# Performance work log

Measured on AMD Instinct MI355X. Metric: run time of the kernel, lower is better.

The kernel has to match this reference:

```python
import jax, jax.numpy as jnp
import numpy as np
import math

B, S, HID = 1, 2048, 4096
NH, NKV, HD = 32, 8, 128
N_REP = NH // NKV
ROPE_THETA = 10000.0


def setup_inputs() -> dict:
    key = jax.random.key(0)
    ks = jax.random.split(key, 5)
    hidden_states = jax.random.normal(ks[0], (B, S, HID), dtype=jnp.float32)
    # additive causal mask: 0 on/below diagonal, -1e9 above
    causal = jnp.triu(jnp.full((S, S), -1e9, dtype=jnp.float32), k=1)
    attention_mask = causal[None, None, :, :]
    wq = jax.random.normal(ks[1], (HID, NH * HD), dtype=jnp.float32) * 0.02
    wk = jax.random.normal(ks[2], (HID, NKV * HD), dtype=jnp.float32) * 0.02
    wv = jax.random.normal(ks[3], (HID, NKV * HD), dtype=jnp.float32) * 0.02
    wo = jax.random.normal(ks[4], (NH * HD, HID), dtype=jnp.float32) * 0.02
    return {"hidden_states": hidden_states, "attention_mask": attention_mask,
            "wq": wq, "wk": wk, "wv": wv, "wo": wo}


def _rope_cos_sin(seq_len, head_dim, base, dtype):
    inv_freq = 1.0 / (base ** (jnp.arange(0, head_dim, 2, dtype=jnp.float32) / head_dim))
    t = jnp.arange(seq_len, dtype=jnp.float32)
    freqs = jnp.outer(t, inv_freq)          # [S, HD/2]
    emb = jnp.concatenate([freqs, freqs], axis=-1)  # [S, HD]
    return jnp.cos(emb).astype(dtype), jnp.sin(emb).astype(dtype)


def _rotate_interleaved(x):
    # pairs (x0,x1) -> (-x1, x0), interleaved (matches torch stack/reshape trick)
    xp = x.reshape(*x.shape[:-1], -1, 2)
    return jnp.stack([-xp[..., 1], xp[..., 0]], axis=-1).reshape(x.shape)


def reference(hidden_states, attention_mask, wq, wk, wv, wo):
    b, s, _ = hidden_states.shape
    q = (hidden_states @ wq).reshape(b, s, NH, HD).transpose(0, 2, 1, 3)   # [B,NH,S,HD]
    k = (hidden_states @ wk).reshape(b, s, NKV, HD).transpose(0, 2, 1, 3)  # [B,NKV,S,HD]
    v = (hidden_states @ wv).reshape(b, s, NKV, HD).transpose(0, 2, 1, 3)

    cos, sin = _rope_cos_sin(s, HD, ROPE_THETA, hidden_states.dtype)
    cos = cos[None, None, :, :]  # broadcast over batch and heads
    sin = sin[None, None, :, :]
    q = q * cos + _rotate_interleaved(q) * sin
    k = k * cos + _rotate_interleaved(k) * sin

    # repeat_kv: [B,NKV,S,HD] -> [B,NH,S,HD]
    k = jnp.repeat(k, N_REP, axis=1)
    v = jnp.repeat(v, N_REP, axis=1)

    scores = jnp.einsum('bhqd,bhkd->bhqk', q, k) / math.sqrt(HD)
    scores = scores + attention_mask
    attn = jax.nn.softmax(scores.astype(jnp.float32), axis=-1).astype(q.dtype)
    out = jnp.einsum('bhqk,bhkd->bhqd', attn, v)          # [B,NH,S,HD]
    out = out.transpose(0, 2, 1, 3).reshape(b, s, NH * HD)
    return out @ wo
```

## Files before the change

### kernel.cpp

```cpp
#include <hip/hip_runtime.h>

#define S_LEN 2048
#define HID 4096
#define NH 32
#define NKV 8
#define HD 128
#define KVW 1024
#define NQKV 6144

typedef _Float16 f16;
typedef _Float16 f16x8 __attribute__((ext_vector_type(8)));
typedef _Float16 f16x4 __attribute__((ext_vector_type(4)));
typedef float f32x4 __attribute__((ext_vector_type(4)));
typedef float f32x16 __attribute__((ext_vector_type(16)));
typedef unsigned int u32;
typedef u32 u32x4 __attribute__((ext_vector_type(4)));

__device__ __forceinline__ void gll16(const void* g, void* lds) {
  __builtin_amdgcn_global_load_lds((const __attribute__((address_space(1))) void*)g,
                                   (__attribute__((address_space(3))) void*)lds, 16, 0, 0);
}

template<int N> __device__ __forceinline__ void vmwait() {
  if constexpr (N == 0) asm volatile("s_waitcnt vmcnt(0)" ::: "memory");
  else if constexpr (N == 3) asm volatile("s_waitcnt vmcnt(3)" ::: "memory");
  else if constexpr (N == 4) asm volatile("s_waitcnt vmcnt(4)" ::: "memory");
  else static_assert(N == 0 || N == 3 || N == 4, "add vmcnt case");
}

__global__ void k_cast(const float* __restrict__ src, f16* __restrict__ dst) {
  size_t i = ((size_t)blockIdx.x * blockDim.x + threadIdx.x) * 8;
  float4 a = *(const float4*)(src + i);
  float4 b = *(const float4*)(src + i + 4);
  f16x8 o = { (f16)a.x, (f16)a.y, (f16)a.z, (f16)a.w,
              (f16)b.x, (f16)b.y, (f16)b.z, (f16)b.w };
  *(f16x8*)(dst + i) = o;
}

__global__ void k_trig(float4* __restrict__ trig) {
  int id = blockIdx.x * blockDim.x + threadIdx.x;
  int s = id >> 6, i = id & 63;
  int j0 = 2 * i, j1 = 2 * i + 1;
  float f0 = powf(10000.f, -(float)(j0 & 63) / 64.f);
  float f1 = powf(10000.f, -(float)(j1 & 63) / 64.f);
  float a0 = (float)s * f0, a1 = (float)s * f1;
  trig[id] = make_float4(cosf(a0), cosf(a1), sinf(a0), sinf(a1));
}

__global__ __launch_bounds__(256) void k_wprep(
    const float* __restrict__ wq, const float* __restrict__ wk,
    const float* __restrict__ wv, const float* __restrict__ wo,
    f16* __restrict__ Wt, f16* __restrict__ Wot)
{
  __shared__ float tile[32][33];
  int bid = blockIdx.x;
  const float* src; f16* dst; int N; int r;
  if (bid < 16384)      { src = wq; dst = Wt;                          N = 4096; r = bid; }
  else if (bid < 20480) { src = wk; dst = Wt + (size_t)4096 * 4096;    N = 1024; r = bid - 16384; }
  else if (bid < 24576) { src = wv; dst = Wt + (size_t)5120 * 4096;    N = 1024; r = bid - 20480; }
  else                  { src = wo; dst = Wot;                         N = 4096; r = bid - 24576; }
  int tpr = N >> 5;
  int kb = (r / tpr) * 32, nb = (r % tpr) * 32;
  int t = threadIdx.x;
  {
    int kl = t >> 3, ng = t & 7;
    float4 v = *(const float4*)(src + (size_t)(kb + kl) * N + nb + ng * 4);
    tile[kl][ng * 4 + 0] = v.x; tile[kl][ng * 4 + 1] = v.y;
    tile[kl][ng * 4 + 2] = v.z; tile[kl][ng * 4 + 3] = v.w;
  }
  __syncthreads();
  {
    int nl = t >> 3, kg = t & 7;
    f16x4 o = { (f16)tile[kg * 4 + 0][nl], (f16)tile[kg * 4 + 1][nl],
                (f16)tile[kg * 4 + 2][nl], (f16)tile[kg * 4 + 3][nl] };
    *(f16x4*)(dst + (size_t)(nb + nl) * HID + kb + kg * 4) = o;
  }
}

extern __shared__ char smem[];

template<int MODE, int MF, int NF, int WM, int WN>
__global__ __launch_bounds__(WM * WN * 64, 2) void k_gemm4(
    const f16* __restrict__ A, const f16* __restrict__ Bt,
    f16* __restrict__ Qr, f16* __restrict__ Kr, f16* __restrict__ Vt,
    const float4* __restrict__ trig, float* __restrict__ Cout)
{
  constexpr int NTHR = WM * WN * 64;
  constexpr int BM = WM * MF * 16;
  constexpr int BN = WN * NF * 16;
  constexpr int ABYTES = BM * 128;
  constexpr int BBYTES = BN * 128;
  constexpr int RPC = NTHR / 8;
  constexpr int ACALLS = BM / RPC;
  constexpr int BCALLS = BN / RPC;
  constexpr int NT = 64;

  const int tid = threadIdx.x, ln = tid & 63, w = tid >> 6;
  const int la = ln & 15, lg = ln >> 4;
  const int wr = w / WN, wc = w % WN;
  const int m0 = blockIdx.y * BM, n0 = blockIdx.x * BN;

  const char* asrc[ACALLS];
  const char* bsrc[BCALLS];
  int adst[ACALLS > BCALLS ? ACALLS : BCALLS];
#pragma unroll
  for (int c = 0; c < ACALLS; ++c) {
    int r = c * RPC + (tid >> 3);
    int g = (tid & 7) ^ (r & 7);
    asrc[c] = (const char*)A + ((size_t)(m0 + r) * HID + (size_t)g * 8) * 2;
    adst[c] = c * NTHR * 16 + tid * 16;
  }
#pragma unroll
  for (int c = 0; c < BCALLS; ++c) {
    int r = c * RPC + (tid >> 3);
    int g = (tid & 7) ^ (r & 7);
    bsrc[c] = (const char*)Bt + ((size_t)(n0 + (r >= BN ? r - BN : r)) * HID + (size_t)g * 8) * 2;
  }

  char* const Bbase = smem + 2 * ABYTES;
  f32x4 acc[MF][NF] = {};

#pragma unroll
  for (int c = 0; c < ACALLS; ++c) gll16(asrc[c], smem + adst[c]);
#pragma unroll
  for (int c = 0; c < BCALLS; ++c) gll16(bsrc[c], Bbase + adst[c]);
#pragma unroll
  for (int c = 0; c < BCALLS; ++c) gll16(bsrc[c] + 128, Bbase + BBYTES + adst[c]);
  vmwait<BCALLS>();
  __builtin_amdgcn_s_barrier();

  for (int t = 0; t < NT; ++t) {
    if (t + 1 < NT) {
      char* sa = smem + ((t + 1) & 1) * ABYTES;
#pragma unroll
      for (int c = 0; c < ACALLS; ++c) gll16(asrc[c] + (size_t)(t + 1) * 128, sa + adst[c]);
    }
    if (t + 2 < NT) {
      char* sb = Bbase + ((t + 2) % 3) * BBYTES;
#pragma unroll
      for (int c = 0; c < BCALLS; ++c) gll16(bsrc[c] + (size_t)(t + 2) * 128, sb + adst[c]);
    }
    const char* sa = smem + (t & 1) * ABYTES;
    const char* sb = Bbase + (t % 3) * BBYTES;
#pragma unroll
    for (int ks = 0; ks < 2; ++ks) {
      f16x8 af[MF], bf[NF];
#pragma unroll
      for (int i = 0; i < MF; ++i) {
        int rl = wr * MF * 16 + i * 16 + la;
        af[i] = *(const f16x8*)(sa + rl * 128 + (((ks * 4 + lg) ^ (rl & 7)) * 16));
      }
#pragma unroll
      for (int n = 0; n < NF; ++n) {
        int rb = wc * NF * 16 + n * 16 + la;
        bf[n] = *(const f16x8*)(sb + rb * 128 + (((ks * 4 + lg) ^ (rb & 7)) * 16));
      }
      __builtin_amdgcn_s_setprio(1);
#pragma unroll
      for (int i = 0; i < MF; ++i)
#pragma unroll
        for (int n = 0; n < NF; ++n)
          acc[i][n] = __builtin_amdgcn_mfma_f32_16x16x32_f16(af[i], bf[n], acc[i][n], 0, 0, 0);
      __builtin_amdgcn_s_setprio(0);
    }
    if (t < NT - 2)      vmwait<BCALLS>();
    else if (t == NT - 2) vmwait<0>();
    if (t < NT - 1) __builtin_amdgcn_s_barrier();
  }

#pragma unroll
  for (int mi = 0; mi < MF; ++mi) {
#pragma unroll
    for (int nf = 0; nf < NF; ++nf) {
      f32x4 fr = acc[mi][nf];
      int n = n0 + wc * NF * 16 + nf * 16 + la;
      int mr = m0 + wr * MF * 16 + mi * 16 + lg * 4;
      if (MODE == 0) {
        if (n < HID + KVW) {
          int d = n & 127;
#pragma unroll
          for (int r = 0; r < 4; ++r) {
            float v = fr[r];
            float p = __shfl_xor(v, 1);
            float4 tc = trig[(size_t)(mr + r) * 64 + (d >> 1)];
            float cv = (d & 1) ? tc.y : tc.x;
            float sv = (d & 1) ? tc.w : tc.z;
            float o = v * cv + ((d & 1) ? p : -p) * sv;
            if (n < HID) Qr[(size_t)(mr + r) * HID + n] = (f16)o;
            else         Kr[(size_t)(mr + r) * KVW + (n - HID)] = (f16)o;
          }
        } else {
          int nv = n - (HID + KVW);
          f16x4 o4 = { (f16)fr[0], (f16)fr[1], (f16)fr[2], (f16)fr[3] };
          *(f16x4*)(Vt + (size_t)nv * S_LEN + mr) = o4;
        }
      } else {
#pragma unroll
        for (int r = 0; r < 4; ++r)
          Cout[(size_t)(mr + r) * HID + n] = fr[r];
      }
    }
  }
}

#define KBYTES (64 * 128 * 2)
#define VBYTES (128 * 64 * 2)

__global__ __launch_bounds__(256, 2) void k_attn(
    const f16* __restrict__ Qr, const f16* __restrict__ Kr, const f16* __restrict__ Vt,
    f16* __restrict__ AO)
{
  int bid = blockIdx.x;
  int h, c;
  if (bid < 256) { h = bid >> 3; c = bid & 7; }
  else           { int t = bid - 256; h = t >> 3; c = 15 - (t & 7); }
  const int hkv = h >> 2;
  const int q0c = c * 128;
  const int NT = 2 * c + 2;

  __shared__ char KV[2][KBYTES + VBYTES];

  const int tid = threadIdx.x;
  const int ln = tid & 63, w = tid >> 6;
  const int q = ln & 31;
  const int hi = ln >> 5;
  const int qg = q0c + w * 32 + q;

  size_t ksrc[4], vsrc[4];
  int kdo[4], vdo[4];
#pragma unroll
  for (int j = 0; j < 4; ++j) {
    int kc = w * 4 + j;
    int kr = kc * 4 + (ln >> 4);
    ksrc[j] = ((size_t)kr * KVW + hkv * HD) * 2 + (size_t)(((ln & 15) ^ (kr & 7)) * 16);
    kdo[j] = kc * 1024;
    int vc = w * 4 + j;
    int d = vc * 8 + (ln >> 3);
    vsrc[j] = ((size_t)(hkv * HD + d) * S_LEN) * 2 + (size_t)(((ln & 7) ^ (d & 7)) * 16);
    vdo[j] = KBYTES + vc * 1024;
  }

  f16x8 qf[8];
  {
    const f16* qrow = Qr + (size_t)qg * HID + h * HD + hi * 8;
#pragma unroll
    for (int ks = 0; ks < 8; ++ks) qf[ks] = *(const f16x8*)(qrow + ks * 16);
  }

  f32x16 ot[4] = {};
  float m2 = -3.0e38f, l = 0.f;
  const float K2 = 0.12753256471f;

  int buf = 0;
#pragma unroll
  for (int j = 0; j < 4; ++j) {
    gll16((const char*)Kr + ksrc[j], &KV[0][kdo[j]]);
    gll16((const char*)Vt + vsrc[j], &KV[0][vdo[j]]);
  }

  for (int jt = 0; jt < NT; ++jt) {
    __syncthreads();
    if (jt + 1 < NT) {
      size_t ko = (size_t)(jt + 1) * 64 * KVW * 2;
      size_t vo = (size_t)(jt + 1) * 64 * 2;
#pragma unroll
      for (int j = 0; j < 4; ++j) {
        gll16((const char*)Kr + ksrc[j] + ko, &KV[buf ^ 1][kdo[j]]);
        gll16((const char*)Vt + vsrc[j] + vo, &KV[buf ^ 1][vdo[j]]);
      }
    }
    const int j0 = jt * 64;
    if (j0 <= q0c + w * 32 + 31) {
      const f16* Kb = (const f16*)&KV[buf][0];
      const f16* Vb = (const f16*)&KV[buf][KBYTES];
      f32x16 s0 = {}, s1 = {};
#pragma unroll
      for (int ks = 0; ks < 8; ++ks) {
        int cc = ((ks * 2 + hi) ^ (q & 7)) * 8;
        f16x8 k0 = *(const f16x8*)(Kb + q * 128 + cc);
        f16x8 k1 = *(const f16x8*)(Kb + (q + 32) * 128 + cc);
        s0 = __builtin_amdgcn_mfma_f32_32x32x16_f16(k0, qf[ks], s0, 0, 0, 0);
        s1 = __builtin_amdgcn_mfma_f32_32x32x16_f16(k1, qf[ks], s1, 0, 0, 0);
      }
      const bool nm = (j0 + 63 > q0c + w * 32);
      float p0[16], p1[16];
      float mx = -3.0e38f;
#pragma unroll
      for (int r = 0; r < 16; ++r) {
        float a = s0[r], b = s1[r];
        if (nm) {
          int kvb = j0 + (r & 3) + 8 * (r >> 2) + 4 * hi;
          if (kvb > qg) a = -3.0e38f;
          if (kvb + 32 > qg) b = -3.0e38f;
        }
        p0[r] = a; p1[r] = b;
        mx = fmaxf(mx, fmaxf(a, b));
      }
      mx = fmaxf(mx, __shfl_xor(mx, 32));
      float m2c = mx * K2;
      int defer = (m2c <= m2 + 11.0f);
      if (!__all(defer)) {
        float m2n = fmaxf(m2, m2c);
        float corr = exp2f(m2 - m2n);
        m2 = m2n; l *= corr;
#pragma unroll
        for (int t = 0; t < 4; ++t)
#pragma unroll
          for (int r = 0; r < 16; ++r) ot[t][r] *= corr;
      }
      float sum = 0.f;
#pragma unroll
      for (int r = 0; r < 16; ++r) {
        p0[r] = exp2f(__builtin_fmaf(p0[r], K2, -m2));
        p1[r] = exp2f(__builtin_fmaf(p1[r], K2, -m2));
        sum += p0[r] + p1[r];
      }
      l += sum + __shfl_xor(sum, 32);
      u32 pw0[8], pw1[8];
#pragma unroll
      for (int t = 0; t < 8; ++t) {
        pw0[t] = __builtin_bit_cast(u32, __builtin_amdgcn_cvt_pkrtz(p0[2 * t], p0[2 * t + 1]));
        pw1[t] = __builtin_bit_cast(u32, __builtin_amdgcn_cvt_pkrtz(p1[2 * t], p1[2 * t + 1]));
      }
      f16x8 pf[4];
#pragma unroll
      for (int ch = 0; ch < 2; ++ch) {
        const u32* pw = ch ? pw1 : pw0;
        u32 sx[8];
#pragma unroll
        for (int t = 0; t < 8; ++t) sx[t] = (u32)__shfl_xor((int)pw[t], 32);
        u32x4 fa = { hi ? sx[2] : pw[0], hi ? sx[3] : pw[1],
                     hi ? pw[2] : sx[0], hi ? pw[3] : sx[1] };
        u32x4 fb = { hi ? sx[6] : pw[4], hi ? sx[7] : pw[5],
                     hi ? pw[6] : sx[4], hi ? pw[7] : sx[5] };
        pf[ch * 2 + 0] = __builtin_bit_cast(f16x8, fa);
        pf[ch * 2 + 1] = __builtin_bit_cast(f16x8, fb);
      }
#pragma unroll
      for (int dt = 0; dt < 4; ++dt) {
        int d = dt * 32 + q;
#pragma unroll
        for (int f = 0; f < 4; ++f) {
          f16x8 vf = *(const f16x8*)(Vb + d * 64 + (((f * 2 + hi) ^ (q & 7)) * 8));
          ot[dt] = __builtin_amdgcn_mfma_f32_32x32x16_f16(vf, pf[f], ot[dt], 0, 0, 0);
        }
      }
    }
    buf ^= 1;
  }

  __syncthreads();
  char* scr = &KV[0][0] + w * 8192;
  float inv = 1.f / l;
#pragma unroll
  for (int dt = 0; dt < 4; ++dt) {
#pragma unroll
    for (int rg = 0; rg < 4; ++rg) {
      u32 wa = __builtin_bit_cast(u32, __builtin_amdgcn_cvt_pkrtz(ot[dt][rg * 4 + 0] * inv, ot[dt][rg * 4 + 1] * inv));
      u32 wb = __builtin_bit_cast(u32, __builtin_amdgcn_cvt_pkrtz(ot[dt][rg * 4 + 2] * inv, ot[dt][rg * 4 + 3] * inv));
      int byte = q * 256 + (((dt * 4 + rg) ^ (q & 7)) * 16) + hi * 8;
      u32* p = (u32*)(scr + byte);
      p[0] = wa; p[1] = wb;
    }
  }
  asm volatile("s_waitcnt lgkmcnt(0)" ::: "memory");
#pragma unroll
  for (int ps = 0; ps < 8; ++ps) {
    int qr = ps * 4 + (ln >> 4);
    int ck = (ln & 15) ^ (qr & 7);
    f16x8 v = *(const f16x8*)(scr + qr * 256 + ck * 16);
    *(f16x8*)(AO + (size_t)(q0c + w * 32 + qr) * HID + h * HD + (ln & 15) * 8) = v;
  }
}

extern "C" void kernel_launch(void* const* d_in, const int* in_sizes, int n_in,
                              void* d_out, int out_size, void* d_ws, size_t ws_size,
                              hipStream_t stream) {
  const float* hs = (const float*)d_in[0];
  const float* wq = (const float*)d_in[2];
  const float* wk = (const float*)d_in[3];
  const float* wv = (const float*)d_in[4];
  const float* wo = (const float*)d_in[5];
  float* out = (float*)d_out;

  char* ws = (char*)d_ws;
  size_t off = 0;
  auto alloc = [&](size_t b) { char* p = ws + off; off += (b + 255) & ~(size_t)255; return p; };
  f16* Hh   = (f16*)alloc((size_t)S_LEN * HID * 2);
  f16* Wt   = (f16*)alloc((size_t)NQKV * HID * 2);
  float4* trig = (float4*)alloc((size_t)S_LEN * 64 * sizeof(float4));
  f16* Qrp  = (f16*)alloc((size_t)S_LEN * HID * 2);
  f16* Krp  = (f16*)alloc((size_t)S_LEN * KVW * 2);
  f16* Vtp  = (f16*)alloc((size_t)KVW * S_LEN * 2);
  f16* AO   = (f16*)alloc((size_t)S_LEN * HID * 2);
  f16* Wot  = (f16*)alloc((size_t)HID * HID * 2);

  hipFuncSetAttribute((const void*)k_gemm4<0, 8, 3, 2, 4>,
                      hipFuncAttributeMaxDynamicSharedMemorySize, 139264);
  hipFuncSetAttribute((const void*)k_gemm4<1, 4, 4, 2, 2>,
                      hipFuncAttributeMaxDynamicSharedMemorySize, 81920);

  k_cast<<<(S_LEN * HID) / (256 * 8), 256, 0, stream>>>(hs, Hh);
  k_trig<<<(S_LEN * 64) / 256, 256, 0, stream>>>(trig);
  k_wprep<<<40960, 256, 0, stream>>>(wq, wk, wv, wo, Wt, Wot);
  k_gemm4<0, 8, 3, 2, 4><<<dim3(NQKV / 192, S_LEN / 256), 512, 139264, stream>>>(
      Hh, Wt, Qrp, Krp, Vtp, trig, nullptr);
  k_attn<<<dim3(512), 256, 0, stream>>>(Qrp, Krp, Vtp, AO);
  k_gemm4<1, 4, 4, 2, 2><<<dim3(HID / 128, S_LEN / 128), 256, 81920, stream>>>(
      AO, Wot, nullptr, nullptr, nullptr, nullptr, out);
}
```

Before: 332.4 us.

## Switch GEMMs to 32x32x16 MFMA with new LDS swizzle and block-order remap

```diff
diff --git a/kernel.cpp b/kernel.cpp
--- a/kernel.cpp
+++ b/kernel.cpp
@@ -79,15 +79,15 @@
 
 extern __shared__ char smem[];
 
-template<int MODE, int MF, int NF, int WM, int WN>
-__global__ __launch_bounds__(WM * WN * 64, 2) void k_gemm4(
+template<int MODE, int MB, int NFB, int WM, int WN>
+__global__ __launch_bounds__(WM * WN * 64, 2) void k_gemm6(
     const f16* __restrict__ A, const f16* __restrict__ Bt,
     f16* __restrict__ Qr, f16* __restrict__ Kr, f16* __restrict__ Vt,
     const float4* __restrict__ trig, float* __restrict__ Cout)
 {
   constexpr int NTHR = WM * WN * 64;
-  constexpr int BM = WM * MF * 16;
-  constexpr int BN = WN * NF * 16;
+  constexpr int BM = WM * MB * 32;
+  constexpr int BN = WN * NFB * 32;
   constexpr int ABYTES = BM * 128;
   constexpr int BBYTES = BN * 128;
   constexpr int RPC = NTHR / 8;
@@ -96,9 +96,18 @@
   constexpr int NT = 64;
 
   const int tid = threadIdx.x, ln = tid & 63, w = tid >> 6;
-  const int la = ln & 15, lg = ln >> 4;
+  const int l31 = ln & 31, hi = ln >> 5;
   const int wr = w / WN, wc = w % WN;
-  const int m0 = blockIdx.y * BM, n0 = blockIdx.x * BN;
+
+  int bx, by;
+  {
+    int gx = gridDim.x;
+    int lin = blockIdx.y * gx + blockIdx.x;
+    int cpx = (gx * gridDim.y) >> 3;
+    int swz = (lin & 7) * cpx + (lin >> 3);
+    by = swz / gx; bx = swz % gx;
+  }
+  const int m0 = by * BM, n0 = bx * BN;
 
   const char* asrc[ACALLS];
   const char* bsrc[BCALLS];
@@ -106,19 +115,19 @@
 #pragma unroll
   for (int c = 0; c < ACALLS; ++c) {
     int r = c * RPC + (tid >> 3);
-    int g = (tid & 7) ^ (r & 7);
+    int g = (tid & 7) ^ (r & 7) ^ ((r >> 3) & 3);
     asrc[c] = (const char*)A + ((size_t)(m0 + r) * HID + (size_t)g * 8) * 2;
     adst[c] = c * NTHR * 16 + tid * 16;
   }
 #pragma unroll
   for (int c = 0; c < BCALLS; ++c) {
     int r = c * RPC + (tid >> 3);
-    int g = (tid & 7) ^ (r & 7);
-    bsrc[c] = (const char*)Bt + ((size_t)(n0 + (r >= BN ? r - BN : r)) * HID + (size_t)g * 8) * 2;
+    int g = (tid & 7) ^ (r & 7) ^ ((r >> 3) & 3);
+    bsrc[c] = (const char*)Bt + ((size_t)(n0 + r) * HID + (size_t)g * 8) * 2;
   }
 
   char* const Bbase = smem + 2 * ABYTES;
-  f32x4 acc[MF][NF] = {};
+  f32x16 acc[MB][NFB] = {};
 
 #pragma unroll
   for (int c = 0; c < ACALLS; ++c) gll16(asrc[c], smem + adst[c]);
@@ -143,24 +152,26 @@
     const char* sa = smem + (t & 1) * ABYTES;
     const char* sb = Bbase + (t % 3) * BBYTES;
 #pragma unroll
-    for (int ks = 0; ks < 2; ++ks) {
-      f16x8 af[MF], bf[NF];
-#pragma unroll
-      for (int i = 0; i < MF; ++i) {
-        int rl = wr * MF * 16 + i * 16 + la;
-        af[i] = *(const f16x8*)(sa + rl * 128 + (((ks * 4 + lg) ^ (rl & 7)) * 16));
-      }
-#pragma unroll
-      for (int n = 0; n < NF; ++n) {
-        int rb = wc * NF * 16 + n * 16 + la;
-        bf[n] = *(const f16x8*)(sb + rb * 128 + (((ks * 4 + lg) ^ (rb & 7)) * 16));
+    for (int kk = 0; kk < 4; ++kk) {
+      f16x8 af[MB], bf[NFB];
+#pragma unroll
+      for (int i = 0; i < MB; ++i) {
+        int rl = wr * (MB * 32) + i * 32 + l31;
+        int s = (kk * 2 + hi) ^ (rl & 7) ^ ((rl >> 3) & 3);
+        af[i] = *(const f16x8*)(sa + rl * 128 + s * 16);
+      }
+#pragma unroll
+      for (int n = 0; n < NFB; ++n) {
+        int rb = wc * (NFB * 32) + n * 32 + l31;
+        int s = (kk * 2 + hi) ^ (rb & 7) ^ ((rb >> 3) & 3);
+        bf[n] = *(const f16x8*)(sb + rb * 128 + s * 16);
       }
       __builtin_amdgcn_s_setprio(1);
 #pragma unroll
-      for (int i = 0; i < MF; ++i)
-#pragma unroll
-        for (int n = 0; n < NF; ++n)
-          acc[i][n] = __builtin_amdgcn_mfma_f32_16x16x32_f16(af[i], bf[n], acc[i][n], 0, 0, 0);
+      for (int i = 0; i < MB; ++i)
+#pragma unroll
+        for (int n = 0; n < NFB; ++n)
+          acc[i][n] = __builtin_amdgcn_mfma_f32_32x32x16_f16(af[i], bf[n], acc[i][n], 0, 0, 0);
       __builtin_amdgcn_s_setprio(0);
     }
     if (t < NT - 2)      vmwait<BCALLS>();
@@ -169,35 +180,40 @@
   }
 
 #pragma unroll
-  for (int mi = 0; mi < MF; ++mi) {
-#pragma unroll
-    for (int nf = 0; nf < NF; ++nf) {
-      f32x4 fr = acc[mi][nf];
-      int n = n0 + wc * NF * 16 + nf * 16 + la;
-      int mr = m0 + wr * MF * 16 + mi * 16 + lg * 4;
-      if (MODE == 0) {
-        if (n < HID + KVW) {
-          int d = n & 127;
-#pragma unroll
-          for (int r = 0; r < 4; ++r) {
-            float v = fr[r];
-            float p = __shfl_xor(v, 1);
-            float4 tc = trig[(size_t)(mr + r) * 64 + (d >> 1)];
-            float cv = (d & 1) ? tc.y : tc.x;
-            float sv = (d & 1) ? tc.w : tc.z;
-            float o = v * cv + ((d & 1) ? p : -p) * sv;
-            if (n < HID) Qr[(size_t)(mr + r) * HID + n] = (f16)o;
-            else         Kr[(size_t)(mr + r) * KVW + (n - HID)] = (f16)o;
+  for (int i = 0; i < MB; ++i) {
+#pragma unroll
+    for (int n = 0; n < NFB; ++n) {
+      f32x16 fr = acc[i][n];
+      int col = n0 + wc * (NFB * 32) + n * 32 + l31;
+      int mbase = m0 + wr * (MB * 32) + i * 32 + 4 * hi;
+#pragma unroll
+      for (int q = 0; q < 4; ++q) {
+        int mr = mbase + q * 8;
+        if (MODE == 0) {
+          if (col < HID + KVW) {
+            int d = col & 127;
+#pragma unroll
+            for (int r = 0; r < 4; ++r) {
+              float v = fr[q * 4 + r];
+              float p = __shfl_xor(v, 1);
+              float4 tc = trig[(size_t)(mr + r) * 64 + (d >> 1)];
+              float cv = (d & 1) ? tc.y : tc.x;
+              float sv = (d & 1) ? tc.w : tc.z;
+              float o = v * cv + ((d & 1) ? p : -p) * sv;
+              if (col < HID) Qr[(size_t)(mr + r) * HID + col] = (f16)o;
+              else           Kr[(size_t)(mr + r) * KVW + (col - HID)] = (f16)o;
+            }
+          } else {
+            int nv = col - (HID + KVW);
+            f16x4 o4 = { (f16)fr[q * 4 + 0], (f16)fr[q * 4 + 1],
+                         (f16)fr[q * 4 + 2], (f16)fr[q * 4 + 3] };
+            *(f16x4*)(Vt + (size_t)nv * S_LEN + mr) = o4;
           }
         } else {
-          int nv = n - (HID + KVW);
-          f16x4 o4 = { (f16)fr[0], (f16)fr[1], (f16)fr[2], (f16)fr[3] };
-          *(f16x4*)(Vt + (size_t)nv * S_LEN + mr) = o4;
+#pragma unroll
+          for (int r = 0; r < 4; ++r)
+            Cout[(size_t)(mr + r) * HID + col] = fr[q * 4 + r];
         }
-      } else {
-#pragma unroll
-        for (int r = 0; r < 4; ++r)
-          Cout[(size_t)(mr + r) * HID + n] = fr[r];
       }
     }
   }
@@ -395,17 +411,17 @@
   f16* AO   = (f16*)alloc((size_t)S_LEN * HID * 2);
   f16* Wot  = (f16*)alloc((size_t)HID * HID * 2);
 
-  hipFuncSetAttribute((const void*)k_gemm4<0, 8, 3, 2, 4>,
+  hipFuncSetAttribute((const void*)k_gemm6<0, 2, 3, 4, 2>,
                       hipFuncAttributeMaxDynamicSharedMemorySize, 139264);
-  hipFuncSetAttribute((const void*)k_gemm4<1, 4, 4, 2, 2>,
+  hipFuncSetAttribute((const void*)k_gemm6<1, 2, 2, 2, 2>,
                       hipFuncAttributeMaxDynamicSharedMemorySize, 81920);
 
   k_cast<<<(S_LEN * HID) / (256 * 8), 256, 0, stream>>>(hs, Hh);
   k_trig<<<(S_LEN * 64) / 256, 256, 0, stream>>>(trig);
   k_wprep<<<40960, 256, 0, stream>>>(wq, wk, wv, wo, Wt, Wot);
-  k_gemm4<0, 8, 3, 2, 4><<<dim3(NQKV / 192, S_LEN / 256), 512, 139264, stream>>>(
+  k_gemm6<0, 2, 3, 4, 2><<<dim3(NQKV / 192, S_LEN / 256), 512, 139264, stream>>>(
       Hh, Wt, Qrp, Krp, Vtp, trig, nullptr);
   k_attn<<<dim3(512), 256, 0, stream>>>(Qrp, Krp, Vtp, AO);
-  k_gemm4<1, 4, 4, 2, 2><<<dim3(HID / 128, S_LEN / 128), 256, 81920, stream>>>(
+  k_gemm6<1, 2, 2, 2, 2><<<dim3(HID / 128, S_LEN / 128), 256, 81920, stream>>>(
       AO, Wot, nullptr, nullptr, nullptr, nullptr, out);
 }
```

Measured after the change: 353.7 us. 1.06x slower.
